# Performance work log

Hardware: AMD Instinct MI355X
Metric: run time of the kernel (lower is better)

The kernel has to match this reference:

```python
import jax, jax.numpy as jnp
import numpy as np

IMG = 16          # imageSize
H = IMG * IMG     # hidden = num_pixels = 256
B = 32768         # batch
LAYERS = 30       # recurrent iterations


def _build_fixed_params():
    """Grid 4-neighbor adjacency + neighbor-count weights (0.25/0.34/0.5)."""
    idx = np.arange(H).reshape(IMG, IMG)
    W = np.zeros((H, H), np.float32)
    for di, dj in ((-1, 0), (1, 0), (0, -1), (0, 1)):
        src = idx[max(0, di):IMG + min(0, di), max(0, dj):IMG + min(0, dj)]
        dst = idx[max(0, -di):IMG + min(0, -di), max(0, -dj):IMG + min(0, -dj)]
        W[src.ravel(), dst.ravel()] = 1.0
    ii, jj = np.meshgrid(np.arange(IMG), np.arange(IMG), indexing='ij')
    on_edge = (ii == 0) | (ii == IMG - 1) | (jj == 0) | (jj == IMG - 1)
    corner = ((ii == 0) | (ii == IMG - 1)) & ((jj == 0) | (jj == IMG - 1))
    w = np.full(H, 0.25, np.float32)
    w[on_edge.ravel()] = 0.34
    w[corner.ravel()] = 0.5
    return W, w


def setup_inputs() -> dict:
    key = jax.random.key(0)
    k1, k2 = jax.random.split(key)
    W_np, w_np = _build_fixed_params()
    return {
        "X": jax.random.normal(k1, (B, H), dtype=jnp.float32),
        "pred": jax.random.normal(k2, (B, H), dtype=jnp.float32),
        "W_hidden": jnp.asarray(W_np),          # [H,H] fixed grid adjacency
        "w": jnp.asarray(w_np),                  # [H] per-row neighbor weight
        "a": jnp.full((H,), 1.0, jnp.float32),   # input gain (inputWeight is identity)
        "bias": jnp.full((H,), -0.15, jnp.float32),
        "scalar": jnp.full((1,), 20.0, jnp.float32),
    }


def reference(X, pred, W_hidden, w, a, bias, scalar):
    # u_fix: initial hidden with -1 entries zeroed (kept fixed across iterations)
    u_fix = jnp.where(pred == -1.0, 0.0, pred)
    Ww = w[:, None] * W_hidden                   # row-scaled adjacency [H,H]
    # inputWeight is the identity matrix, so (a*I) @ x == a * x elementwise
    drive = u_fix + bias[None, :] + a[None, :] * X   # constant per iteration [B,H]

    def step(u, _):
        v = drive + u @ Ww.T                     # [B,H]
        return jnp.tanh(v * scalar), None

    u, _ = jax.lax.scan(step, pred, None, length=LAYERS)
    return u
```

## Files before the change

### kernel.cpp

```cpp
#include <hip/hip_runtime.h>


namespace {

constexpr int HPIX   = 256;
constexpr int LAYERS = 30;
constexpr int WAVES_PER_BLOCK = 4;
constexpr int IMGS_PER_WAVE   = 4;

template <int CTRL>
__device__ __forceinline__ float dppf(float x) {
    int r = __builtin_amdgcn_update_dpp(0, __float_as_int(x), CTRL, 0xF, 0xF, true);
    return __int_as_float(r);
}

__global__ __launch_bounds__(WAVES_PER_BLOCK * 64)
void pp_kernel(const float* __restrict__ X, const float* __restrict__ pred,
               const float* __restrict__ w, const float* __restrict__ av,
               const float* __restrict__ bias, const float* __restrict__ scalar,
               float* __restrict__ out, int nb)
{
    const int lane = threadIdx.x & 63;
    const int wid  = blockIdx.x * WAVES_PER_BLOCK + (threadIdx.x >> 6);
    const int g    = lane >> 4;
    const int r    = lane & 15;
    const int img  = wid * IMGS_PER_WAVE + g;
    const bool act = (img < nb);
    const int imgc = act ? img : 0;
    const size_t base = (size_t)imgc * HPIX + r * 16;
    const int    prow = r * 16;

    const float s = scalar[0];
    const float K = 2.0f * s * 1.4426950408889634f;

    float u[16], drv[16];
#pragma unroll
    for (int k = 0; k < 4; ++k) {
        const float4 x4 = *reinterpret_cast<const float4*>(X    + base + k * 4);
        const float4 p4 = *reinterpret_cast<const float4*>(pred + base + k * 4);
        const float4 b4 = *reinterpret_cast<const float4*>(bias + prow + k * 4);
        const float4 a4 = *reinterpret_cast<const float4*>(av   + prow + k * 4);
        const float px[4] = {p4.x, p4.y, p4.z, p4.w};
        const float xx[4] = {x4.x, x4.y, x4.z, x4.w};
        const float bb[4] = {b4.x, b4.y, b4.z, b4.w};
        const float aa[4] = {a4.x, a4.y, a4.z, a4.w};
#pragma unroll
        for (int j = 0; j < 4; ++j) {
            const int c = k * 4 + j;
            const float pr   = px[j];
            const float ufix = (pr == -1.0f) ? 0.0f : pr;
            drv[c] = K * ((ufix + bb[j]) + aa[j] * xx[j]);
            u[c]   = pr;
        }
    }
    const float w2b = K * w[prow];
    const float w2a = K * w[prow + 1];

#pragma unroll 1
    for (int it = 0; it < LAYERS; ++it) {
        float ns[16];
        ns[0]  = u[1];
        ns[15] = u[14];
#pragma unroll
        for (int c = 1; c < 15; ++c) ns[c] = u[c - 1] + u[c + 1];
#pragma unroll
        for (int c = 0; c < 16; ++c)
            ns[c] = ns[c] + dppf<0x111>(u[c]) + dppf<0x101>(u[c]);
#pragma unroll
        for (int c = 0; c < 16; ++c) {
            const float wc = (c == 0 || c == 15) ? w2b : w2a;
            const float m  = __builtin_fmaf(wc, ns[c], drv[c]);
            const float e  = __builtin_amdgcn_exp2f(m);
            const float rd = __builtin_amdgcn_rcpf(e + 1.0f);
            u[c] = __builtin_fmaf(rd, -2.0f, 1.0f);
        }
    }

    if (act) {
#pragma unroll
        for (int k = 0; k < 4; ++k) {
            float4 o4;
            o4.x = u[k * 4 + 0]; o4.y = u[k * 4 + 1];
            o4.z = u[k * 4 + 2]; o4.w = u[k * 4 + 3];
            *reinterpret_cast<float4*>(out + base + k * 4) = o4;
        }
    }
}

}

extern "C" void kernel_launch(void* const* d_in, const int* in_sizes, int n_in,
                              void* d_out, int out_size, void* d_ws, size_t ws_size,
                              hipStream_t stream) {
    const float* X      = (const float*)d_in[0];
    const float* pred   = (const float*)d_in[1];
    const float* w      = (const float*)d_in[3];
    const float* av     = (const float*)d_in[4];
    const float* bias   = (const float*)d_in[5];
    const float* scalar = (const float*)d_in[6];
    float* out = (float*)d_out;

    const int nb = in_sizes[0] / HPIX;
    const int imgs_per_block = WAVES_PER_BLOCK * IMGS_PER_WAVE;
    const int blocks = (nb + imgs_per_block - 1) / imgs_per_block;

    pp_kernel<<<dim3(blocks), dim3(WAVES_PER_BLOCK * 64), 0, stream>>>(
        X, pred, w, av, bias, scalar, out, nb);
}
```

Baseline: 72.64 us.

## Process two images per lane with packed fp32 math and Newton-based tanh

Each lane now holds two images in 2-wide float vectors, and the images per wave double. The intent is for the compiler to emit packed fp32 FMA/add instructions and to gain instruction-level parallelism. The tanh is rebuilt from exp2 of a negative absolute value plus a three-step Newton reciprocal, with the sign restored by copysign. This replaces the transcendental rcp with VALU work. The stencil update is also streamed in place, carrying the previous column in a register. The cost is a larger register footprint, half as many waves, and extra ALU ops for the Newton iterations.

```diff
diff --git a/kernel.cpp b/kernel.cpp
--- a/kernel.cpp
+++ b/kernel.cpp
@@ -6,12 +6,40 @@
 constexpr int HPIX   = 256;
 constexpr int LAYERS = 30;
 constexpr int WAVES_PER_BLOCK = 4;
-constexpr int IMGS_PER_WAVE   = 4;
+constexpr int IMGS_PER_WAVE   = 8;
+
+typedef float v2f __attribute__((ext_vector_type(2)));
 
 template <int CTRL>
 __device__ __forceinline__ float dppf(float x) {
     int r = __builtin_amdgcn_update_dpp(0, __float_as_int(x), CTRL, 0xF, 0xF, true);
     return __int_as_float(r);
+}
+
+__device__ __forceinline__ v2f vert_add(v2f ns, v2f uc) {
+    ns.x += dppf<0x111>(uc.x) + dppf<0x101>(uc.x);
+    ns.y += dppf<0x111>(uc.y) + dppf<0x101>(uc.y);
+    return ns;
+}
+
+__device__ __forceinline__ v2f act(v2f ns, v2f drv, v2f wc) {
+    const v2f m = wc * ns + drv;
+    v2f am;
+    am.x = __builtin_fabsf(m.x);
+    am.y = __builtin_fabsf(m.y);
+    v2f e;
+    e.x = __builtin_amdgcn_exp2f(-am.x);
+    e.y = __builtin_amdgcn_exp2f(-am.y);
+    const v2f d = e + 1.0f;
+    v2f r = d * (-8.0f / 17.0f) + (24.0f / 17.0f);
+    r = r * (2.0f - d * r);
+    r = r * (2.0f - d * r);
+    r = r * (2.0f - d * r);
+    const v2f t = 1.0f - 2.0f * (e * r);
+    v2f u;
+    u.x = __builtin_copysignf(t.x, m.x);
+    u.y = __builtin_copysignf(t.y, m.y);
+    return u;
 }
 
 __global__ __launch_bounds__(WAVES_PER_BLOCK * 64)
@@ -24,65 +52,82 @@
     const int wid  = blockIdx.x * WAVES_PER_BLOCK + (threadIdx.x >> 6);
     const int g    = lane >> 4;
     const int r    = lane & 15;
-    const int img  = wid * IMGS_PER_WAVE + g;
-    const bool act = (img < nb);
-    const int imgc = act ? img : 0;
-    const size_t base = (size_t)imgc * HPIX + r * 16;
-    const int    prow = r * 16;
+    const int imgA = wid * IMGS_PER_WAVE + g * 2;
+    const bool act0 = (imgA < nb);
+    const bool act1 = (imgA + 1 < nb);
+    const int iA = act0 ? imgA : 0;
+    const int iB = act1 ? imgA + 1 : 0;
+    const size_t baseA = (size_t)iA * HPIX + r * 16;
+    const size_t baseB = (size_t)iB * HPIX + r * 16;
+    const int    prow  = r * 16;
 
     const float s = scalar[0];
     const float K = 2.0f * s * 1.4426950408889634f;
 
-    float u[16], drv[16];
+    v2f u[16], drv[16];
 #pragma unroll
     for (int k = 0; k < 4; ++k) {
-        const float4 x4 = *reinterpret_cast<const float4*>(X    + base + k * 4);
-        const float4 p4 = *reinterpret_cast<const float4*>(pred + base + k * 4);
+        const float4 xA = *reinterpret_cast<const float4*>(X    + baseA + k * 4);
+        const float4 xB = *reinterpret_cast<const float4*>(X    + baseB + k * 4);
+        const float4 pA = *reinterpret_cast<const float4*>(pred + baseA + k * 4);
+        const float4 pB = *reinterpret_cast<const float4*>(pred + baseB + k * 4);
         const float4 b4 = *reinterpret_cast<const float4*>(bias + prow + k * 4);
         const float4 a4 = *reinterpret_cast<const float4*>(av   + prow + k * 4);
-        const float px[4] = {p4.x, p4.y, p4.z, p4.w};
-        const float xx[4] = {x4.x, x4.y, x4.z, x4.w};
+        const float xa[4] = {xA.x, xA.y, xA.z, xA.w};
+        const float xb[4] = {xB.x, xB.y, xB.z, xB.w};
+        const float pa[4] = {pA.x, pA.y, pA.z, pA.w};
+        const float pb[4] = {pB.x, pB.y, pB.z, pB.w};
         const float bb[4] = {b4.x, b4.y, b4.z, b4.w};
         const float aa[4] = {a4.x, a4.y, a4.z, a4.w};
 #pragma unroll
         for (int j = 0; j < 4; ++j) {
             const int c = k * 4 + j;
-            const float pr   = px[j];
-            const float ufix = (pr == -1.0f) ? 0.0f : pr;
-            drv[c] = K * ((ufix + bb[j]) + aa[j] * xx[j]);
-            u[c]   = pr;
+            const float ua = pa[j], ub = pb[j];
+            const float fa = (ua == -1.0f) ? 0.0f : ua;
+            const float fb = (ub == -1.0f) ? 0.0f : ub;
+            drv[c].x = K * ((fa + bb[j]) + aa[j] * xa[j]);
+            drv[c].y = K * ((fb + bb[j]) + aa[j] * xb[j]);
+            u[c].x = ua;
+            u[c].y = ub;
         }
     }
-    const float w2b = K * w[prow];
-    const float w2a = K * w[prow + 1];
+    const float wbs = K * w[prow];
+    const float was = K * w[prow + 1];
+    const v2f w2b = {wbs, wbs};
+    const v2f w2a = {was, was};
 
 #pragma unroll 1
     for (int it = 0; it < LAYERS; ++it) {
-        float ns[16];
-        ns[0]  = u[1];
-        ns[15] = u[14];
+        v2f uprev = u[0];
+        {
+            v2f ns = vert_add(u[1], u[0]);
+            u[0] = act(ns, drv[0], w2b);
+        }
 #pragma unroll
-        for (int c = 1; c < 15; ++c) ns[c] = u[c - 1] + u[c + 1];
-#pragma unroll
-        for (int c = 0; c < 16; ++c)
-            ns[c] = ns[c] + dppf<0x111>(u[c]) + dppf<0x101>(u[c]);
-#pragma unroll
-        for (int c = 0; c < 16; ++c) {
-            const float wc = (c == 0 || c == 15) ? w2b : w2a;
-            const float m  = __builtin_fmaf(wc, ns[c], drv[c]);
-            const float e  = __builtin_amdgcn_exp2f(m);
-            const float rd = __builtin_amdgcn_rcpf(e + 1.0f);
-            u[c] = __builtin_fmaf(rd, -2.0f, 1.0f);
+        for (int c = 1; c < 15; ++c) {
+            v2f ns = vert_add(uprev + u[c + 1], u[c]);
+            uprev = u[c];
+            u[c] = act(ns, drv[c], w2a);
+        }
+        {
+            v2f ns = vert_add(uprev, u[15]);
+            u[15] = act(ns, drv[15], w2b);
         }
     }
 
-    if (act) {
 #pragma unroll
-        for (int k = 0; k < 4; ++k) {
-            float4 o4;
-            o4.x = u[k * 4 + 0]; o4.y = u[k * 4 + 1];
-            o4.z = u[k * 4 + 2]; o4.w = u[k * 4 + 3];
-            *reinterpret_cast<float4*>(out + base + k * 4) = o4;
+    for (int k = 0; k < 4; ++k) {
+        if (act0) {
+            float4 oA;
+            oA.x = u[k * 4 + 0].x; oA.y = u[k * 4 + 1].x;
+            oA.z = u[k * 4 + 2].x; oA.w = u[k * 4 + 3].x;
+            *reinterpret_cast<float4*>(out + baseA + k * 4) = oA;
+        }
+        if (act1) {
+            float4 oB;
+            oB.x = u[k * 4 + 0].y; oB.y = u[k * 4 + 1].y;
+            oB.z = u[k * 4 + 2].y; oB.w = u[k * 4 + 3].y;
+            *reinterpret_cast<float4*>(out + baseB + k * 4) = oB;
         }
     }
 }
```

New measurement: 107.3 us. +47.7%, slower.

## Remap lanes to columns with split row halves, exchanging boundary rows via bpermute

Applied to the files above, without the earlier changes.

Each 64-lane wave now handles two images instead of four. Each lane owns one column and eight rows, and the image is split across two 16-lane groups, so the vertical-neighbour boundary row is exchanged with ds_bpermute. Loads and stores become per-column scalar accesses that coalesce across lanes, replacing float4 row loads. The aim is to double the number of waves and halve the register footprint per lane for more parallelism. The cost is an LDS-crossbar permute every iteration and scalar rather than vector memory accesses.

```diff
diff --git a/kernel.cpp b/kernel.cpp
--- a/kernel.cpp
+++ b/kernel.cpp
@@ -6,7 +6,7 @@
 constexpr int HPIX   = 256;
 constexpr int LAYERS = 30;
 constexpr int WAVES_PER_BLOCK = 4;
-constexpr int IMGS_PER_WAVE   = 4;
+constexpr int IMGS_PER_WAVE   = 2;
 
 template <int CTRL>
 __device__ __forceinline__ float dppf(float x) {
@@ -22,68 +22,65 @@
 {
     const int lane = threadIdx.x & 63;
     const int wid  = blockIdx.x * WAVES_PER_BLOCK + (threadIdx.x >> 6);
-    const int g    = lane >> 4;
-    const int r    = lane & 15;
+    const int g    = lane >> 5;
+    const int rg   = (lane >> 4) & 1;
+    const int c    = lane & 15;
     const int img  = wid * IMGS_PER_WAVE + g;
-    const bool act = (img < nb);
-    const int imgc = act ? img : 0;
-    const size_t base = (size_t)imgc * HPIX + r * 16;
-    const int    prow = r * 16;
+    const bool active = (img < nb);
+    const int imgc = active ? img : 0;
+    const int r0   = rg * 8;
+    const size_t base = (size_t)imgc * HPIX + r0 * 16 + c;
 
     const float s = scalar[0];
     const float K = 2.0f * s * 1.4426950408889634f;
 
-    float u[16], drv[16];
+    float u[8], drv[8];
 #pragma unroll
-    for (int k = 0; k < 4; ++k) {
-        const float4 x4 = *reinterpret_cast<const float4*>(X    + base + k * 4);
-        const float4 p4 = *reinterpret_cast<const float4*>(pred + base + k * 4);
-        const float4 b4 = *reinterpret_cast<const float4*>(bias + prow + k * 4);
-        const float4 a4 = *reinterpret_cast<const float4*>(av   + prow + k * 4);
-        const float px[4] = {p4.x, p4.y, p4.z, p4.w};
-        const float xx[4] = {x4.x, x4.y, x4.z, x4.w};
-        const float bb[4] = {b4.x, b4.y, b4.z, b4.w};
-        const float aa[4] = {a4.x, a4.y, a4.z, a4.w};
-#pragma unroll
-        for (int j = 0; j < 4; ++j) {
-            const int c = k * 4 + j;
-            const float pr   = px[j];
-            const float ufix = (pr == -1.0f) ? 0.0f : pr;
-            drv[c] = K * ((ufix + bb[j]) + aa[j] * xx[j]);
-            u[c]   = pr;
-        }
+    for (int k = 0; k < 8; ++k) {
+        const int p = r0 * 16 + k * 16 + c;
+        const float pr = pred[base + k * 16];
+        const float x  = X[base + k * 16];
+        const float fu = (pr == -1.0f) ? 0.0f : pr;
+        drv[k] = K * ((fu + bias[p]) + av[p] * x);
+        u[k]   = pr;
     }
-    const float w2b = K * w[prow];
-    const float w2a = K * w[prow + 1];
+    const float wEnd = K * w[c];
+    const float wMid = K * w[16 + c];
+    const float w_k0 = rg ? wMid : wEnd;
+    const float w_k7 = rg ? wEnd : wMid;
+
+    const int partner_addr = (lane ^ 16) << 2;
 
 #pragma unroll 1
     for (int it = 0; it < LAYERS; ++it) {
-        float ns[16];
-        ns[0]  = u[1];
-        ns[15] = u[14];
+        const float pub = rg ? u[0] : u[7];
+        const float nbr = __int_as_float(
+            __builtin_amdgcn_ds_bpermute(partner_addr, __float_as_int(pub)));
+        const float tN = rg ? nbr : 0.0f;
+        const float bN = rg ? 0.0f : nbr;
+
+        float ns[8];
+        ns[0] = tN + u[1];
+        ns[7] = u[6] + bN;
 #pragma unroll
-        for (int c = 1; c < 15; ++c) ns[c] = u[c - 1] + u[c + 1];
+        for (int k = 1; k < 7; ++k) ns[k] = u[k - 1] + u[k + 1];
 #pragma unroll
-        for (int c = 0; c < 16; ++c)
-            ns[c] = ns[c] + dppf<0x111>(u[c]) + dppf<0x101>(u[c]);
+        for (int k = 0; k < 8; ++k)
+            ns[k] = ns[k] + dppf<0x111>(u[k]) + dppf<0x101>(u[k]);
 #pragma unroll
-        for (int c = 0; c < 16; ++c) {
-            const float wc = (c == 0 || c == 15) ? w2b : w2a;
-            const float m  = __builtin_fmaf(wc, ns[c], drv[c]);
+        for (int k = 0; k < 8; ++k) {
+            const float wc = (k == 0) ? w_k0 : (k == 7) ? w_k7 : wMid;
+            const float m  = __builtin_fmaf(wc, ns[k], drv[k]);
             const float e  = __builtin_amdgcn_exp2f(m);
             const float rd = __builtin_amdgcn_rcpf(e + 1.0f);
-            u[c] = __builtin_fmaf(rd, -2.0f, 1.0f);
+            u[k] = __builtin_fmaf(rd, -2.0f, 1.0f);
         }
     }
 
-    if (act) {
+    if (active) {
 #pragma unroll
-        for (int k = 0; k < 4; ++k) {
-            float4 o4;
-            o4.x = u[k * 4 + 0]; o4.y = u[k * 4 + 1];
-            o4.z = u[k * 4 + 2]; o4.w = u[k * 4 + 3];
-            *reinterpret_cast<float4*>(out + base + k * 4) = o4;
-        }
+        for (int k = 0; k < 8; ++k)
+            out[base + k * 16] = u[k];
     }
 }
 
```

New measurement: 73.27 us. No clear change (+0.9%).
